# Kernel optimization log

Measured on AMD Instinct MI355X. Metric: run time of the kernel, lower is better.

The kernel has to match this reference:

```python
import jax, jax.numpy as jnp
import numpy as np

EPS = 1e-12  # F.normalize default eps


def setup_inputs() -> dict:
    key = jax.random.key(0)
    x = jax.random.normal(key, (10000, 512), dtype=jnp.float32)
    return {"x": x, "k": 9}


def reference(x, k):
    # F.normalize(x, p=2, dim=0): L2-normalize each feature column over points
    col_norm = jnp.sqrt(jnp.sum(x * x, axis=0, keepdims=True))  # [1, D]
    xn = x / jnp.maximum(col_norm, EPS)                          # [N, D]

    # pairwise squared euclidean distance: ||xi||^2 - 2 xi.xj + ||xj||^2
    sq = jnp.sum(xn * xn, axis=-1, keepdims=True)                # [N, 1]
    dist = sq - 2.0 * (xn @ xn.T) + sq.T                          # [N, N]

    # k nearest neighbors = top-k of negative distance
    _, nn_idx = jax.lax.top_k(-dist, k)                           # [N, k] int32

    n = x.shape[0]
    center_idx = jnp.broadcast_to(jnp.arange(n, dtype=nn_idx.dtype)[:, None], (n, k))
    edge_idx = jnp.stack((nn_idx, center_idx), axis=0)            # [2, N, k]
    return edge_idx
```

## Files before the change

kernel.cpp:

```cpp
#include <hip/hip_runtime.h>
#include <math.h>

#define DD 512
#define NBLKA 400

#define PM 128
#define PN 128
#define KB 32
#define CSPLIT 6
#define NC 12
#define PBUF 32
#define PBSTRIDE 36
#define NCTOT (CSPLIT*NC)
#define KOUTMAX 16
#define RS_MARGIN 2e-4f

typedef __attribute__((ext_vector_type(8))) short bf16x8;
typedef __attribute__((ext_vector_type(4))) float f32x4;

static __device__ __forceinline__ unsigned short f2bf(float f) {
    unsigned u = __float_as_uint(f);
    u += 0x7fff + ((u >> 16) & 1);
    return (unsigned short)(u >> 16);
}

__global__ void colsum_partial(const float* __restrict__ x, double* __restrict__ partial,
                               int N, int rows_per_block) {
    int b = blockIdx.x;
    int t = threadIdx.x;
    int r0 = b * rows_per_block;
    int r1 = min(r0 + rows_per_block, N);
    double s0 = 0.0, s1 = 0.0;
    for (int r = r0; r < r1; ++r) {
        float v0 = x[(size_t)r * DD + t];
        float v1 = x[(size_t)r * DD + t + 256];
        s0 += (double)v0 * (double)v0;
        s1 += (double)v1 * (double)v1;
    }
    partial[(size_t)b * DD + t]       = s0;
    partial[(size_t)b * DD + t + 256] = s1;
}

__global__ void colnorm_finish(const double* __restrict__ partial, double* __restrict__ rn,
                               double* __restrict__ w, int nblk) {
    int c = threadIdx.x;
    double s = 0.0;
    for (int b = 0; b < nblk; ++b) s += partial[(size_t)b * DD + c];
    double n = fmax(sqrt(s), 1e-12);
    double r = 1.0 / n;
    rn[c]  = r;
    w[c]   = r * r;
}

__global__ void row_sq(const float* __restrict__ x, const double* __restrict__ rn,
                       double* __restrict__ sq, float* __restrict__ sqf,
                       unsigned short* __restrict__ xnbf, int N) {
    int i = blockIdx.x;
    int t = threadIdx.x;
    double a0 = (double)x[(size_t)i * DD + t]       * rn[t];
    double a1 = (double)x[(size_t)i * DD + t + 256] * rn[t + 256];
    xnbf[(size_t)i * DD + t]       = f2bf((float)a0);
    xnbf[(size_t)i * DD + t + 256] = f2bf((float)a1);
    double local = a0 * a0 + a1 * a1;
    __shared__ double red[256];
    red[t] = local;
    __syncthreads();
    for (int off = 128; off > 0; off >>= 1) {
        if (t < off) red[t] += red[t + off];
        __syncthreads();
    }
    if (t == 0) { sq[i] = red[0]; sqf[i] = (float)red[0]; }
}

__global__ __launch_bounds__(256, 2) void gemm_prefilter(
    const unsigned short* __restrict__ xnbf,
    const float* __restrict__ sqf, int* __restrict__ cand, float* __restrict__ cands,
    int N, int ntileM, int ntileN)
{
    __shared__ __align__(16) unsigned char lds_raw[65536];
    __shared__ float sqi_s[PM];
    __shared__ float sqj_s[PN];
    __shared__ float thr_s[PM];
    __shared__ int   cnt_s[PM];
    __shared__ int   flag_s;

    float (*Bsc)[PBSTRIDE] = (float (*)[PBSTRIDE]) lds_raw;
    int   (*Bid)[PBSTRIDE] = (int   (*)[PBSTRIDE]) (lds_raw + 32768);

    const int bid   = blockIdx.x;
    const int q     = bid & 7;
    const int s     = bid >> 3;
    const int ridx  = s / CSPLIT;
    const int split = s - ridx * CSPLIT;
    const int rowb  = q + 8 * ridx;
    if (rowb >= ntileM) return;
    const int row0  = rowb * PM;

    const int t      = threadIdx.x;
    const int lane   = t & 63;
    const int lane15 = t & 15;
    const int quad   = (t >> 4) & 3;
    const int wave   = t >> 6;
    const int wr     = (wave >> 1) * 64;
    const int wc     = (wave & 1) * 64;
    unsigned char* wreg = lds_raw + (size_t)wave * 16384;
    const int sl     = quad ^ (lane15 & 3);

    if (t == 0) flag_s = 0;
    if (t < PM) {
        int i = row0 + t;
        sqi_s[t] = (i < N) ? sqf[i] : 0.f;
        thr_s[t] = __builtin_inff();
        cnt_s[t] = 0;
    }

    float ls[NC];
    int   li[NC];
#pragma unroll
    for (int m = 0; m < NC; ++m) { ls[m] = __builtin_inff(); li[m] = 0x7fffffff; }

    f32x4 acc[4][4];

    for (int tile = split; tile < ntileN; tile += CSPLIT) {
        int col0 = tile * PN;

        if (t < PN) {
            int j = col0 + t;
            sqj_s[t] = (j < N) ? sqf[j] : __builtin_inff();
        }
        __syncthreads();

#pragma unroll
        for (int mt = 0; mt < 4; ++mt)
#pragma unroll
            for (int nt = 0; nt < 4; ++nt)
                acc[mt][nt] = (f32x4){0.f, 0.f, 0.f, 0.f};

        auto STAGE = [&](int kc, int h) {
            unsigned char* base = wreg + (size_t)h * 8192;
#pragma unroll
            for (int l = 0; l < 4; ++l) {
                int e = l * 64 + lane;
                int r = e >> 2;
                int c = (e & 3) ^ (r & 3);
                size_t gA = (size_t)(row0 + wr + r) * DD + kc + c * 8;
                __builtin_amdgcn_global_load_lds(
                    (const unsigned int*)(xnbf + gA),
                    (unsigned int*)(base + (size_t)e * 16), 16, 0, 0);
                size_t gB = (size_t)(col0 + wc + r) * DD + kc + c * 8;
                __builtin_amdgcn_global_load_lds(
                    (const unsigned int*)(xnbf + gB),
                    (unsigned int*)(base + 4096 + (size_t)e * 16), 16, 0, 0);
            }
        };

        STAGE(0, 0);
#pragma unroll 1
        for (int cc = 0; cc < 16; ++cc) {
            if (cc < 15) {
                STAGE((cc + 1) * KB, (cc + 1) & 1);
                __builtin_amdgcn_sched_barrier(0);
                asm volatile("s_waitcnt vmcnt(8)" ::: "memory");
            } else {
                __builtin_amdgcn_sched_barrier(0);
                asm volatile("s_waitcnt vmcnt(0)" ::: "memory");
            }
            __builtin_amdgcn_sched_barrier(0);

            const unsigned char* rb = wreg + (size_t)(cc & 1) * 8192;
            bf16x8 af[4], bfg[4];
#pragma unroll
            for (int mt = 0; mt < 4; ++mt)
                af[mt] = *(const bf16x8*)(rb + ((size_t)((mt * 16 + lane15) * 4 + sl)) * 16);
#pragma unroll
            for (int nt = 0; nt < 4; ++nt)
                bfg[nt] = *(const bf16x8*)(rb + 4096 + ((size_t)((nt * 16 + lane15) * 4 + sl)) * 16);
#pragma unroll
            for (int mt = 0; mt < 4; ++mt)
#pragma unroll
                for (int nt = 0; nt < 4; ++nt)
                    acc[mt][nt] = __builtin_amdgcn_mfma_f32_16x16x32_bf16(
                        af[mt], bfg[nt], acc[mt][nt], 0, 0, 0);
            __builtin_amdgcn_sched_barrier(0);
        }

#pragma unroll
        for (int mt = 0; mt < 4; ++mt)
#pragma unroll
            for (int nt = 0; nt < 4; ++nt)
#pragma unroll
                for (int reg = 0; reg < 4; ++reg) {
                    int rl = wr + mt * 16 + quad * 4 + reg;
                    int cl = wc + nt * 16 + lane15;
                    float g = acc[mt][nt][reg];
                    acc[mt][nt][reg] = (sqi_s[rl] - 2.f * g) + sqj_s[cl];
                }
        __syncthreads();

        bool tile_edge = (col0 + PN > N);
        unsigned long long done = 0ull;
        for (;;) {
#pragma unroll
            for (int mt = 0; mt < 4; ++mt)
#pragma unroll
                for (int reg = 0; reg < 4; ++reg) {
                    const unsigned long long gb =
                        (0x1111ull << reg) << (mt * 16);
                    int rl = wr + mt * 16 + quad * 4 + reg;
                    float th = thr_s[rl];
                    float gmin = fminf(fminf(acc[mt][0][reg], acc[mt][1][reg]),
                                       fminf(acc[mt][2][reg], acc[mt][3][reg]));
                    if (!tile_edge && gmin > th) { done |= gb; continue; }
                    if ((done & gb) == gb) continue;
#pragma unroll
                    for (int nt = 0; nt < 4; ++nt) {
                        const unsigned long long bit = 1ull << (mt * 16 + nt * 4 + reg);
                        if (!(done & bit)) {
                            float sv = acc[mt][nt][reg];
                            int   j  = col0 + wc + nt * 16 + lane15;
                            if (j < N && sv <= th) {
                                int pos = atomicAdd(&cnt_s[rl], 1);
                                if (pos < PBUF) {
                                    Bsc[rl][pos] = sv;
                                    Bid[rl][pos] = j;
                                    done |= bit;
                                }
                            } else {
                                done |= bit;
                            }
                        }
                    }
                }
            if (done != ~0ull) flag_s = 1;
            __syncthreads();
            if (t < PM) {
                int c = cnt_s[t];
                if (c > PBUF) c = PBUF;
                cnt_s[t] = 0;
                for (int m0 = 0; m0 < c; m0 += 4) {
                    float4 s4 = *(const float4*)&Bsc[t][m0];
                    int4   j4 = *(const int4*)&Bid[t][m0];
#pragma unroll
                    for (int e = 0; e < 4; ++e) {
                        if (m0 + e >= c) break;
                        float sv = (e == 0) ? s4.x : (e == 1) ? s4.y : (e == 2) ? s4.z : s4.w;
                        int   j  = (e == 0) ? j4.x : (e == 1) ? j4.y : (e == 2) ? j4.z : j4.w;
                        if (sv < ls[NC - 1] || (sv == ls[NC - 1] && j < li[NC - 1])) {
                            float cs = sv; int cj = j;
#pragma unroll
                            for (int p = 0; p < NC; ++p) {
                                bool lt = (cs < ls[p]) || (cs == ls[p] && cj < li[p]);
                                float ts = ls[p]; int tj = li[p];
                                if (lt) { ls[p] = cs; li[p] = cj; cs = ts; cj = tj; }
                            }
                        }
                    }
                }
                thr_s[t] = ls[NC - 1];
            }
            __syncthreads();
            int go = flag_s;
            __syncthreads();
            if (t == 0) flag_s = 0;
            __syncthreads();
            if (!go) break;
        }
    }
    if (t < PM) {
        int i = row0 + t;
        if (i < N) {
#pragma unroll
            for (int m = 0; m < NC; ++m) {
                cand [(size_t)i * NCTOT + split * NC + m] = li[m];
                cands[(size_t)i * NCTOT + split * NC + m] = ls[m];
            }
        }
    }
}

__global__ __launch_bounds__(256) void rescore_topk(
    const float* __restrict__ x, const double* __restrict__ w,
    const double* __restrict__ sq, const int* __restrict__ cand,
    const float* __restrict__ cands, int* __restrict__ out, int N, int k)
{
    __shared__ float Ssc[4][NCTOT];
    int lane = threadIdx.x & 63;
    int wid  = threadIdx.x >> 6;
    int i = blockIdx.x * 4 + wid;
    if (i >= N) return;

    size_t base = (size_t)i * NCTOT;
    Ssc[wid][lane] = cands[base + lane];
    if (lane < NCTOT - 64) Ssc[wid][64 + lane] = cands[base + 64 + lane];

    float p0 = Ssc[wid][lane];
    float p1 = Ssc[wid][64 + (lane & 7)];
    int c0 = 0, c1 = 0;
    for (int m = 0; m < NCTOT; ++m) {
        float s = Ssc[wid][m];
        c0 += (s <= p0); c1 += (s <= p1);
    }
    float best = __builtin_inff();
    if (c0 >= k) best = p0;
    if (c1 >= k && p1 < best) best = p1;
#pragma unroll
    for (int off = 32; off > 0; off >>= 1)
        best = fminf(best, __shfl_xor(best, off, 64));
    float cut = best + RS_MARGIN;

    double aw[8];
#pragma unroll
    for (int c = 0; c < 8; ++c) {
        int d = lane + 64 * c;
        aw[c] = (double)x[(size_t)i * DD + d] * w[d];
    }
    double sqi = sq[i];

    double bs[KOUTMAX];
    int    bj[KOUTMAX];
    for (int r = 0; r < k; ++r) { bs[r] = __builtin_inf(); bj[r] = 0x7fffffff; }

    int pend = -1;
    for (int m = 0; m <= NCTOT; ++m) {
        int j1cand = -1;
        if (m < NCTOT) {
            if (Ssc[wid][m] > cut) continue;
            j1cand = cand[base + m];
            if (pend < 0) { pend = j1cand; continue; }
        } else if (pend < 0) {
            break;
        }
        int j0 = pend, j1 = j1cand;
        pend = -1;
        const float* q0 = &x[(size_t)j0 * DD + lane];
        const float* q1 = (j1 >= 0) ? &x[(size_t)j1 * DD + lane] : q0;
        float v0[8], v1[8];
#pragma unroll
        for (int c = 0; c < 8; ++c) v0[c] = q0[64 * c];
#pragma unroll
        for (int c = 0; c < 8; ++c) v1[c] = q1[64 * c];
        double d0 = 0.0, d1 = 0.0;
#pragma unroll
        for (int c = 0; c < 8; ++c) d0 = fma(aw[c], (double)v0[c], d0);
#pragma unroll
        for (int c = 0; c < 8; ++c) d1 = fma(aw[c], (double)v1[c], d1);
#pragma unroll
        for (int off = 32; off > 0; off >>= 1) {
            d0 += __shfl_xor(d0, off, 64);
            d1 += __shfl_xor(d1, off, 64);
        }
        double s0 = (sqi - 2.0 * d0) + sq[j0];
        double s1 = (j1 >= 0) ? (sqi - 2.0 * d1) + sq[j1] : __builtin_inf();
#pragma unroll 1
        for (int pick = 0; pick < 2; ++pick) {
            double sv = pick ? s1 : s0;
            int    j  = pick ? j1 : j0;
            if (j < 0) continue;
            if (sv < bs[k - 1] || (sv == bs[k - 1] && j < bj[k - 1])) {
                int pos = k - 1;
                while (pos > 0) {
                    double ps = bs[pos - 1]; int pj = bj[pos - 1];
                    if (!(sv < ps || (sv == ps && j < pj))) break;
                    bs[pos] = ps; bj[pos] = pj;
                    --pos;
                }
                bs[pos] = sv; bj[pos] = j;
            }
        }
    }
    if (lane == 0) {
        for (int r = 0; r < k; ++r) {
            out[(size_t)i * k + r]                 = bj[r];
            out[(size_t)N * k + (size_t)i * k + r] = i;
        }
    }
}

extern "C" void kernel_launch(void* const* d_in, const int* in_sizes, int n_in,
                              void* d_out, int out_size, void* d_ws, size_t ws_size,
                              hipStream_t stream) {
    const float* x = (const float*)d_in[0];
    int N = in_sizes[0] / DD;
    int k = out_size / (2 * N);
    if (k > KOUTMAX) k = KOUTMAX;

    char* ws = (char*)d_ws;
    double*         partial = (double*)ws;
    double*         rn      = (double*)(ws + 1638400);
    double*         w       = (double*)(ws + 1642496);
    double*         sq      = (double*)(ws + 1646592);
    float*          sqf     = (float*) (ws + 1726592);
    unsigned short* xnbf    = (unsigned short*)(ws + 1766592);
    int*            cand    = (int*)   (ws + 12006592);
    float*          cands   = (float*) (ws + 14886592);

    int rpb = (N + NBLKA - 1) / NBLKA;
    hipLaunchKernelGGL(colsum_partial, dim3(NBLKA), dim3(256), 0, stream, x, partial, N, rpb);
    hipLaunchKernelGGL(colnorm_finish, dim3(1), dim3(512), 0, stream, partial, rn, w, NBLKA);
    hipLaunchKernelGGL(row_sq, dim3(N), dim3(256), 0, stream, x, rn, sq, sqf, xnbf, N);

    int ntileM = (N + PM - 1) / PM;
    int ntileN = (N + PN - 1) / PN;
    int rows_per_xcd = (ntileM + 7) / 8;
    int nblk = 8 * rows_per_xcd * CSPLIT;
    hipLaunchKernelGGL(gemm_prefilter, dim3(nblk), dim3(256), 0, stream,
                       xnbf, sqf, cand, cands, N, ntileM, ntileN);

    hipLaunchKernelGGL(rescore_topk, dim3((N + 3) / 4), dim3(256), 0, stream,
                       x, w, sq, cand, cands, (int*)d_out, N, k);
}
```

Before: 802.2 us.

## Share staged GEMM tiles block-wide with 4-deep prefetch; one wave per row in row_sq

The GEMM prefilter stops having each wave stage its own private copy of its A/B sub-tiles. The block now cooperatively stages the full 128x32 A and B tiles into a shared 4-buffer LDS ring, prefetching three K-chunks ahead with a block barrier each step. This removes duplicate global loads across waves and deepens latency hiding, at the cost of a per-iteration s_barrier. row_sq is also rewritten to handle one row per wave with float4 loads and a shuffle reduction, replacing the shared-memory tree reduction.

```diff
diff --git a/kernel.cpp b/kernel.cpp
--- a/kernel.cpp
+++ b/kernel.cpp
@@ -52,24 +52,37 @@
     w[c]   = r * r;
 }
 
-__global__ void row_sq(const float* __restrict__ x, const double* __restrict__ rn,
+__global__ __launch_bounds__(256) void row_sq(const float* __restrict__ x,
+                       const double* __restrict__ rn,
                        double* __restrict__ sq, float* __restrict__ sqf,
                        unsigned short* __restrict__ xnbf, int N) {
-    int i = blockIdx.x;
-    int t = threadIdx.x;
-    double a0 = (double)x[(size_t)i * DD + t]       * rn[t];
-    double a1 = (double)x[(size_t)i * DD + t + 256] * rn[t + 256];
-    xnbf[(size_t)i * DD + t]       = f2bf((float)a0);
-    xnbf[(size_t)i * DD + t + 256] = f2bf((float)a1);
-    double local = a0 * a0 + a1 * a1;
-    __shared__ double red[256];
-    red[t] = local;
-    __syncthreads();
-    for (int off = 128; off > 0; off >>= 1) {
-        if (t < off) red[t] += red[t + off];
-        __syncthreads();
-    }
-    if (t == 0) { sq[i] = red[0]; sqf[i] = (float)red[0]; }
+    int lane = threadIdx.x & 63;
+    int wid  = threadIdx.x >> 6;
+    int i = blockIdx.x * 4 + wid;
+    if (i >= N) return;
+
+    const float4* xr = (const float4*)(x + (size_t)i * DD);
+    float4 v0 = xr[lane];
+    float4 v1 = xr[64 + lane];
+    const double2* rp = (const double2*)rn;
+    double2 r0a = rp[lane * 2],       r0b = rp[lane * 2 + 1];
+    double2 r1a = rp[128 + lane * 2], r1b = rp[128 + lane * 2 + 1];
+
+    double a0 = (double)v0.x * r0a.x, a1 = (double)v0.y * r0a.y;
+    double a2 = (double)v0.z * r0b.x, a3 = (double)v0.w * r0b.y;
+    double b0 = (double)v1.x * r1a.x, b1 = (double)v1.y * r1a.y;
+    double b2 = (double)v1.z * r1b.x, b3 = (double)v1.w * r1b.y;
+
+    ushort4 s0 = { f2bf((float)a0), f2bf((float)a1), f2bf((float)a2), f2bf((float)a3) };
+    ushort4 s1 = { f2bf((float)b0), f2bf((float)b1), f2bf((float)b2), f2bf((float)b3) };
+    *(ushort4*)(xnbf + (size_t)i * DD + lane * 4)       = s0;
+    *(ushort4*)(xnbf + (size_t)i * DD + 256 + lane * 4) = s1;
+
+    double loc = a0*a0 + a1*a1 + a2*a2 + a3*a3 + b0*b0 + b1*b1 + b2*b2 + b3*b3;
+#pragma unroll
+    for (int off = 32; off > 0; off >>= 1)
+        loc += __shfl_xor(loc, off, 64);
+    if (lane == 0) { sq[i] = loc; sqf[i] = (float)loc; }
 }
 
 __global__ __launch_bounds__(256, 2) void gemm_prefilter(
@@ -97,13 +110,11 @@
     const int row0  = rowb * PM;
 
     const int t      = threadIdx.x;
-    const int lane   = t & 63;
     const int lane15 = t & 15;
     const int quad   = (t >> 4) & 3;
     const int wave   = t >> 6;
     const int wr     = (wave >> 1) * 64;
     const int wc     = (wave & 1) * 64;
-    unsigned char* wreg = lds_raw + (size_t)wave * 16384;
     const int sl     = quad ^ (lane15 & 3);
 
     if (t == 0) flag_s = 0;
@@ -136,45 +147,42 @@
             for (int nt = 0; nt < 4; ++nt)
                 acc[mt][nt] = (f32x4){0.f, 0.f, 0.f, 0.f};
 
-        auto STAGE = [&](int kc, int h) {
-            unsigned char* base = wreg + (size_t)h * 8192;
+        auto STAGE = [&](int kc, int buf) {
 #pragma unroll
             for (int l = 0; l < 4; ++l) {
-                int e = l * 64 + lane;
-                int r = e >> 2;
-                int c = (e & 3) ^ (r & 3);
-                size_t gA = (size_t)(row0 + wr + r) * DD + kc + c * 8;
+                int e      = t + l * 256;
+                int region = e >> 9;
+                int re     = e & 511;
+                int row    = re >> 2;
+                int c      = (re & 3) ^ (row & 3);
+                int basei  = region ? col0 : row0;
+                size_t g = (size_t)(basei + row) * DD + kc + c * 8;
                 __builtin_amdgcn_global_load_lds(
-                    (const unsigned int*)(xnbf + gA),
-                    (unsigned int*)(base + (size_t)e * 16), 16, 0, 0);
-                size_t gB = (size_t)(col0 + wc + r) * DD + kc + c * 8;
-                __builtin_amdgcn_global_load_lds(
-                    (const unsigned int*)(xnbf + gB),
-                    (unsigned int*)(base + 4096 + (size_t)e * 16), 16, 0, 0);
+                    (const unsigned int*)(xnbf + g),
+                    (unsigned int*)(lds_raw + (size_t)buf * 16384 + (size_t)e * 16), 16, 0, 0);
             }
         };
 
-        STAGE(0, 0);
+        STAGE(0, 0); STAGE(KB, 1); STAGE(2 * KB, 2);
 #pragma unroll 1
         for (int cc = 0; cc < 16; ++cc) {
-            if (cc < 15) {
-                STAGE((cc + 1) * KB, (cc + 1) & 1);
-                __builtin_amdgcn_sched_barrier(0);
-                asm volatile("s_waitcnt vmcnt(8)" ::: "memory");
-            } else {
-                __builtin_amdgcn_sched_barrier(0);
-                asm volatile("s_waitcnt vmcnt(0)" ::: "memory");
-            }
+            if (cc <= 13)      asm volatile("s_waitcnt vmcnt(8)" ::: "memory");
+            else if (cc == 14) asm volatile("s_waitcnt vmcnt(4)" ::: "memory");
+            else               asm volatile("s_waitcnt vmcnt(0)" ::: "memory");
+            __builtin_amdgcn_s_barrier();
             __builtin_amdgcn_sched_barrier(0);
-
-            const unsigned char* rb = wreg + (size_t)(cc & 1) * 8192;
+            if (cc + 3 < 16)
+                STAGE((cc + 3) * KB, (cc + 3) & 3);
+            __builtin_amdgcn_sched_barrier(0);
+
+            const unsigned char* rb = lds_raw + (size_t)(cc & 3) * 16384;
             bf16x8 af[4], bfg[4];
 #pragma unroll
             for (int mt = 0; mt < 4; ++mt)
-                af[mt] = *(const bf16x8*)(rb + ((size_t)((mt * 16 + lane15) * 4 + sl)) * 16);
+                af[mt] = *(const bf16x8*)(rb + (size_t)(wr + mt * 16 + lane15) * 64 + sl * 16);
 #pragma unroll
             for (int nt = 0; nt < 4; ++nt)
-                bfg[nt] = *(const bf16x8*)(rb + 4096 + ((size_t)((nt * 16 + lane15) * 4 + sl)) * 16);
+                bfg[nt] = *(const bf16x8*)(rb + 8192 + (size_t)(wc + nt * 16 + lane15) * 64 + sl * 16);
 #pragma unroll
             for (int mt = 0; mt < 4; ++mt)
 #pragma unroll
@@ -397,7 +405,7 @@
     int rpb = (N + NBLKA - 1) / NBLKA;
     hipLaunchKernelGGL(colsum_partial, dim3(NBLKA), dim3(256), 0, stream, x, partial, N, rpb);
     hipLaunchKernelGGL(colnorm_finish, dim3(1), dim3(512), 0, stream, partial, rn, w, NBLKA);
-    hipLaunchKernelGGL(row_sq, dim3(N), dim3(256), 0, stream, x, rn, sq, sqf, xnbf, N);
+    hipLaunchKernelGGL(row_sq, dim3((N + 3) / 4), dim3(256), 0, stream, x, rn, sq, sqf, xnbf, N);
 
     int ntileM = (N + PM - 1) / PM;
     int ntileN = (N + PN - 1) / PN;
```

New measurement: 800.0 us. Within noise of the previous version (-0.3%).
